# Optimization experiments

Hardware: AMD Instinct MI355X
Metric: run time of the kernel (lower is better)

Reference implementation:

```python
import jax, jax.numpy as jnp
import numpy as np

D_MODEL = 2048
N_HEADS = 16
HEAD_DIM = D_MODEL // N_HEADS
D_FF = 8192


def setup_inputs() -> dict:
    key = jax.random.key(0)
    ks = jax.random.split(key, 16)
    s = 0.02
    inp = {
        'x': jax.random.normal(ks[0], (2, 2048, D_MODEL), dtype=jnp.float32),
        'Wq': jax.random.normal(ks[1], (D_MODEL, D_MODEL), jnp.float32) * s,
        'bq': jnp.zeros((D_MODEL,), jnp.float32),
        'Wk': jax.random.normal(ks[2], (D_MODEL, D_MODEL), jnp.float32) * s,
        'bk': jnp.zeros((D_MODEL,), jnp.float32),
        'Wv': jax.random.normal(ks[3], (D_MODEL, D_MODEL), jnp.float32) * s,
        'bv': jnp.zeros((D_MODEL,), jnp.float32),
        'Wo': jax.random.normal(ks[4], (D_MODEL, D_MODEL), jnp.float32) * s,
        'bo': jnp.zeros((D_MODEL,), jnp.float32),
        'rotary': jax.random.normal(ks[5], (1, 1, HEAD_DIM), jnp.float32) * s,
        'norm1_w': jnp.ones((D_MODEL,), jnp.float32),
        'norm2_w': jnp.ones((D_MODEL,), jnp.float32),
        'W1': jax.random.normal(ks[6], (2 * D_FF, D_MODEL), jnp.float32) * s,
        'b1': jnp.zeros((2 * D_FF,), jnp.float32),
        'W2': jax.random.normal(ks[7], (D_MODEL, D_FF), jnp.float32) * s,
        'b2': jnp.zeros((D_MODEL,), jnp.float32),
    }
    return inp


def _rmsnorm(x, w, eps=1e-8):
    return w * (x * jax.lax.rsqrt(jnp.mean(x * x, axis=-1, keepdims=True) + eps))


def reference(x, Wq, bq, Wk, bk, Wv, bv, Wo, bo, rotary, norm1_w, norm2_w, W1, b1, W2, b2):
    B, S, _ = x.shape
    # --- attention block ---
    h = _rmsnorm(x, norm1_w)
    q = (h @ Wq.T + bq).reshape(B, S, N_HEADS, HEAD_DIM)
    k = (h @ Wk.T + bk).reshape(B, S, N_HEADS, HEAD_DIM)
    v = (h @ Wv.T + bv).reshape(B, S, N_HEADS, HEAD_DIM)
    q = q + rotary  # (1,1,head_dim) broadcast over batch, seq, heads
    scores = jnp.einsum('bqhd,bkhd->bhqk', q, k) / jnp.sqrt(jnp.float32(HEAD_DIM))
    attn = jax.nn.softmax(scores, axis=-1)
    o = jnp.einsum('bhqk,bkhd->bqhd', attn, v).reshape(B, S, D_MODEL)
    x = x + (o @ Wo.T + bo)
    # --- SwiGLU FFN block ---
    h2 = _rmsnorm(x, norm2_w)
    g = h2 @ W1.T + b1
    x1, x2 = g[..., :D_FF], g[..., D_FF:]
    ff = (x1 * jax.nn.silu(x2)) @ W2.T + b2
    return x + ff
```

## Files before the change

### kernel.cpp

```cpp
#include <hip/hip_runtime.h>
#include <hip/hip_bf16.h>

#define D_MODEL 2048
#define N_HEADS 16
#define HEAD_DIM 128
#define D_FF 8192
#define BATCH 2
#define SEQ 2048
#define M_TOK (BATCH * SEQ)
#define QKV_LD 6144
#define QSCALE 0.12751744f

typedef __attribute__((ext_vector_type(8))) short short8;
typedef __attribute__((ext_vector_type(4))) short short4v;
typedef __attribute__((ext_vector_type(4))) float f32x4;
typedef __attribute__((ext_vector_type(16))) float f32x16;
typedef __attribute__((ext_vector_type(2))) unsigned int uint2v;
typedef __attribute__((ext_vector_type(4))) unsigned int uint4v;

__device__ __forceinline__ unsigned short f2b(float f) {
  __hip_bfloat16 h = __float2bfloat16(f);
  return *reinterpret_cast<unsigned short*>(&h);
}
__device__ __forceinline__ float b2f(unsigned short u) {
  unsigned int x = ((unsigned int)u) << 16;
  return __uint_as_float(x);
}

__device__ __forceinline__ void gload_lds16(const void* gsrc, void* ldst) {
  __builtin_amdgcn_global_load_lds(
      (const __attribute__((address_space(1))) void*)gsrc,
      (__attribute__((address_space(3))) void*)ldst, 16, 0, 0);
}

__device__ __forceinline__ f32x16 mfma32(short8 a, short8 b, f32x16 c) {
  return __builtin_amdgcn_mfma_f32_32x32x16_bf16(a, b, c, 0, 0, 0);
}
__device__ __forceinline__ unsigned int cvtpk(float lo, float hi) {
  unsigned int r;
  asm("v_cvt_pk_bf16_f32 %0, %1, %2" : "=v"(r) : "v"(lo), "v"(hi));
  return r;
}
__device__ __forceinline__ uint2v plswap(unsigned int a, unsigned int b) {
  return __builtin_amdgcn_permlane32_swap(a, b, false, false);
}

__global__ __launch_bounds__(256)
void cvt_kernel(const float* __restrict__ src, unsigned short* __restrict__ dst,
                int nchunks, float scale) {
  int i = blockIdx.x * blockDim.x + threadIdx.x;
  int stride = gridDim.x * blockDim.x;
  for (int c = i; c < nchunks; c += stride) {
    const float4 a = *(const float4*)(src + (size_t)c * 8);
    const float4 b = *(const float4*)(src + (size_t)c * 8 + 4);
    short8 r;
    r[0] = f2b(a.x * scale); r[1] = f2b(a.y * scale);
    r[2] = f2b(a.z * scale); r[3] = f2b(a.w * scale);
    r[4] = f2b(b.x * scale); r[5] = f2b(b.y * scale);
    r[6] = f2b(b.z * scale); r[7] = f2b(b.w * scale);
    *(short8*)(dst + (size_t)c * 8) = r;
  }
}

__global__ __launch_bounds__(256)
void cvt_w1p_kernel(const float* __restrict__ src,
                    unsigned short* __restrict__ dst) {
  int i = blockIdx.x * blockDim.x + threadIdx.x;
  int stride = gridDim.x * blockDim.x;
  const int total = 2 * D_FF * (D_MODEL / 8);
  for (int c = i; c < total; c += stride) {
    int rp = c >> 8, col8 = c & 255;
    int b = rp >> 6, half = (rp >> 5) & 1;
    int rs = half * D_FF + b * 32 + (rp & 31);
    const float* s = src + (size_t)rs * D_MODEL + col8 * 8;
    const float4 a = *(const float4*)s;
    const float4 bb = *(const float4*)(s + 4);
    short8 r;
    r[0] = f2b(a.x); r[1] = f2b(a.y); r[2] = f2b(a.z); r[3] = f2b(a.w);
    r[4] = f2b(bb.x); r[5] = f2b(bb.y); r[6] = f2b(bb.z); r[7] = f2b(bb.w);
    *(short8*)(dst + (size_t)c * 8) = r;
  }
}

__global__ void permb1_kernel(const float* __restrict__ b1,
                              float* __restrict__ b1p) {
  int i = blockIdx.x * 256 + threadIdx.x;
  int b = i >> 6, half = (i >> 5) & 1;
  b1p[i] = b1[half * D_FF + b * 32 + (i & 31)];
}

__global__ void biasqkv_kernel(const float* __restrict__ bq,
                               const float* __restrict__ bk,
                               const float* __restrict__ bv,
                               const float* __restrict__ rot,
                               float* __restrict__ outp) {
  int i = blockIdx.x * 256 + threadIdx.x;
  float v;
  if (i < 2048) v = (bq[i] + rot[i & (HEAD_DIM - 1)]) * QSCALE;
  else if (i < 4096) v = bk[i - 2048];
  else v = bv[i - 4096];
  outp[i] = v;
}

__global__ __launch_bounds__(256)
void rmsnorm_kernel(const float* __restrict__ x, const float* __restrict__ wv,
                    unsigned short* __restrict__ outp) {
  const int row = blockIdx.x;
  const float* xr = x + (size_t)row * D_MODEL;
  const int base = threadIdx.x * 8;
  float4 a = *(const float4*)(xr + base);
  float4 c = *(const float4*)(xr + base + 4);
  float ss = a.x * a.x + a.y * a.y + a.z * a.z + a.w * a.w +
             c.x * c.x + c.y * c.y + c.z * c.z + c.w * c.w;
#pragma unroll
  for (int m = 1; m < 64; m <<= 1) ss += __shfl_xor(ss, m);
  __shared__ float red[4];
  if ((threadIdx.x & 63) == 0) red[threadIdx.x >> 6] = ss;
  __syncthreads();
  float tot = red[0] + red[1] + red[2] + red[3];
  float sc = rsqrtf(tot * (1.0f / D_MODEL) + 1e-8f);
  float4 w0 = *(const float4*)(wv + base);
  float4 w1 = *(const float4*)(wv + base + 4);
  short8 r;
  r[0] = f2b(a.x * sc * w0.x); r[1] = f2b(a.y * sc * w0.y);
  r[2] = f2b(a.z * sc * w0.z); r[3] = f2b(a.w * sc * w0.w);
  r[4] = f2b(c.x * sc * w1.x); r[5] = f2b(c.y * sc * w1.y);
  r[6] = f2b(c.z * sc * w1.z); r[7] = f2b(c.w * sc * w1.w);
  *(short8*)(outp + (size_t)row * D_MODEL + base) = r;
}

template <int MODE>
__global__ __launch_bounds__(512, 2)
void gemm_p8(const unsigned short* __restrict__ A, int lda,
             const unsigned short* __restrict__ W, int ldw,
             const float* __restrict__ bias, void* __restrict__ outp,
             int N, int K, size_t out_zstride) {
  __shared__ unsigned short AL[2][2][128 * 64];
  __shared__ unsigned short BL[2][2][128 * 64];
  const int t = threadIdx.x;
  const int l = t & 63, w = t >> 6;
  const int wm = w >> 2, wn = w & 3;
  const int ln = l & 31, hi = l >> 5;
  const int m0 = blockIdx.y << 8, n0 = blockIdx.x << 8;
  const int koff = blockIdx.z * K;

  const int r0 = t >> 3;
  const int cb16 = (t & 7) * 16;
  const int sel = ((cb16 ^ ((r0 & 7) << 4)) >> 1);
  const unsigned short* Abase = A + (size_t)m0 * lda + koff;
  const unsigned short* Wbase = W + (size_t)n0 * ldw + koff;
  const int d0e = t * 8, d1e = (t + 512) * 8;

#define STAGE(XL, Xb, ld, dd, h, ktd)                                        \
  do {                                                                       \
    const unsigned short* s_ =                                               \
        (Xb) + (size_t)((h) * 128 + r0) * (ld) + (ktd) * 64 + sel;           \
    gload_lds16(s_, &XL[dd][h][d0e]);                                        \
    gload_lds16(s_ + (size_t)64 * (ld), &XL[dd][h][d1e]);                    \
  } while (0)

  const int swz = (ln & 7) << 4;
  const int hb = wn >> 1;
  const int browb = ((wn & 1) * 64 + ln) * 128;

  f32x16 acc[4][2] = {};
  short8 bf[2][4];

#define READB(dd)                                                            \
  do {                                                                       \
    const char* Bb_ = (const char*)&BL[dd][hb][0];                           \
    _Pragma("unroll") for (int cb_ = 0; cb_ < 2; cb_++)                      \
      _Pragma("unroll") for (int ks_ = 0; ks_ < 4; ks_++)                    \
        bf[cb_][ks_] = *(const short8*)(Bb_ + browb + cb_ * 4096 +           \
                                        ((ks_ * 32 + hi * 16) ^ swz));       \
  } while (0)

#define PHASE2(dd, p, STAGE_STMT, VM_STMT)                                   \
  do {                                                                       \
    const char* Ab_ = (const char*)&AL[dd][p][0];                            \
    short8 af_[2][4];                                                        \
    if ((p) == 0) READB(dd);                                                 \
    _Pragma("unroll") for (int sb_ = 0; sb_ < 2; sb_++) {                    \
      _Pragma("unroll") for (int ks_ = 0; ks_ < 4; ks_++)                    \
        af_[sb_][ks_] = *(const short8*)(Ab_ +                               \
                                         (wm * 64 + sb_ * 32 + ln) * 128 +   \
                                         ((ks_ * 32 + hi * 16) ^ swz));      \
    }                                                                        \
    STAGE_STMT;                                                              \
    __builtin_amdgcn_sched_barrier(0);                                       \
    VM_STMT;                                                                 \
    __builtin_amdgcn_sched_barrier(0);                                       \
    __builtin_amdgcn_s_barrier();                                            \
    __builtin_amdgcn_sched_barrier(0);                                       \
    __builtin_amdgcn_s_setprio(1);                                           \
    _Pragma("unroll") for (int sb_ = 0; sb_ < 2; sb_++)                      \
      _Pragma("unroll") for (int cb_ = 0; cb_ < 2; cb_++)                    \
        _Pragma("unroll") for (int ks_ = 0; ks_ < 4; ks_++)                  \
          acc[2 * (p) + sb_][cb_] =                                          \
              mfma32(af_[sb_][ks_], bf[cb_][ks_], acc[2 * (p) + sb_][cb_]);  \
    __builtin_amdgcn_s_setprio(0);                                           \
    __builtin_amdgcn_sched_barrier(0);                                       \
    __builtin_amdgcn_s_barrier();                                            \
    __builtin_amdgcn_sched_barrier(0);                                       \
  } while (0)

  const int NT = K >> 6;

  STAGE(AL, Abase, lda, 0, 0, 0);
  STAGE(AL, Abase, lda, 0, 1, 0);
  STAGE(BL, Wbase, ldw, 0, 0, 0);
  STAGE(BL, Wbase, ldw, 0, 1, 0);
  STAGE(AL, Abase, lda, 1, 0, 1);
  STAGE(BL, Wbase, ldw, 1, 0, 1);
  asm volatile("s_waitcnt vmcnt(4)" ::: "memory");
  __builtin_amdgcn_sched_barrier(0);
  __builtin_amdgcn_s_barrier();
  __builtin_amdgcn_sched_barrier(0);

  for (int kt = 0; kt < NT; kt += 2) {
    PHASE2(0, 0,
           {
             if (kt + 1 < NT) {
               STAGE(BL, Wbase, ldw, 1, 1, kt + 1);
               STAGE(AL, Abase, lda, 1, 1, kt + 1);
             }
           },
           {});
    PHASE2(0, 1,
           {
             if (kt + 2 < NT) {
               STAGE(AL, Abase, lda, 0, 0, kt + 2);
               STAGE(BL, Wbase, ldw, 0, 0, kt + 2);
             }
           },
           {
             if (kt + 2 < NT)
               asm volatile("s_waitcnt vmcnt(4)" ::: "memory");
             else
               asm volatile("s_waitcnt vmcnt(0)" ::: "memory");
           });
    PHASE2(1, 0,
           {
             if (kt + 2 < NT) {
               STAGE(BL, Wbase, ldw, 0, 1, kt + 2);
               STAGE(AL, Abase, lda, 0, 1, kt + 2);
             }
           },
           {});
    PHASE2(1, 1,
           {
             if (kt + 3 < NT) {
               STAGE(AL, Abase, lda, 1, 0, kt + 3);
               STAGE(BL, Wbase, ldw, 1, 0, kt + 3);
             }
           },
           {
             if (kt + 3 < NT)
               asm volatile("s_waitcnt vmcnt(4)" ::: "memory");
             else
               asm volatile("s_waitcnt vmcnt(0)" ::: "memory");
           });
  }
#undef PHASE2
#undef READB
#undef STAGE

#pragma unroll
  for (int rb = 0; rb < 4; rb++) {
    const int rowb = m0 + (rb >> 1) * 128 + wm * 64 + (rb & 1) * 32 + 4 * hi;
    if (MODE == 3) {
      const int col0 = n0 + wn * 64 + ln;
      const float b1v = bias[col0];
      const float b2v = bias[col0 + 32];
      const int jout = (n0 >> 1) + wn * 32 + ln;
#pragma unroll
      for (int r = 0; r < 16; r++) {
        const int row = rowb + (r & 3) + 8 * (r >> 2);
        float x1 = acc[rb][0][r] + b1v;
        float x2 = acc[rb][1][r] + b2v;
        float sg = x2 * __builtin_amdgcn_rcpf(1.0f + __expf(-x2));
        ((unsigned short*)outp)[(size_t)row * (N >> 1) + jout] = f2b(x1 * sg);
      }
    } else {
#pragma unroll
      for (int cb = 0; cb < 2; cb++) {
        const int col = n0 + wn * 64 + cb * 32 + ln;
        const float bv = (MODE == 0) ? bias[col] : 0.0f;
#pragma unroll
        for (int r = 0; r < 16; r++) {
          const int row = rowb + (r & 3) + 8 * (r >> 2);
          const float vv = acc[rb][cb][r] + bv;
          if (MODE == 0)
            ((unsigned short*)outp)[(size_t)row * N + col] = f2b(vv);
          else
            ((float*)outp + blockIdx.z * out_zstride)[(size_t)row * N + col] = vv;
        }
      }
    }
  }
}

__global__ __launch_bounds__(256)
void vtrans_kernel(const unsigned short* __restrict__ qkv,
                   unsigned short* __restrict__ vt) {
  const int bh = blockIdx.y;
  const int b = bh >> 4, h = bh & 15;
  const int s0 = blockIdx.x * 32;
  __shared__ unsigned short tile[32][136];
  const int t = threadIdx.x;
  for (int i = 0; i < 2; i++) {
    int c = t + i * 256;
    int s = c >> 4, dc = c & 15;
    *(short8*)&tile[s][dc * 8] =
        *(const short8*)(qkv + (size_t)(b * SEQ + s0 + s) * QKV_LD + 4096 +
                         h * HEAD_DIM + dc * 8);
  }
  __syncthreads();
  const int d = t >> 1, sh = (t & 1) * 16;
  unsigned short* dst = vt + ((size_t)bh * HEAD_DIM + d) * SEQ + s0 + sh;
  short8 r0, r1;
#pragma unroll
  for (int j = 0; j < 8; j++) r0[j] = tile[sh + j][d];
#pragma unroll
  for (int j = 0; j < 8; j++) r1[j] = tile[sh + 8 + j][d];
  *(short8*)dst = r0;
  *(short8*)(dst + 8) = r1;
}

__global__ __launch_bounds__(512, 2)
void attn_kernel(const unsigned short* __restrict__ qkv,
                 const unsigned short* __restrict__ vt,
                 unsigned short* __restrict__ o) {
  const int bh = blockIdx.y;
  const int b = bh >> 4, h = bh & 15;
  const int q0 = blockIdx.x << 8;
  const int t = threadIdx.x, w = t >> 6, l = t & 63;
  const int ln = l & 31, hi = l >> 5;

  __shared__ unsigned short Ks[2][64 * 128];

  short8 qf[8];
  {
    const unsigned short* qb =
        qkv + (size_t)(b * SEQ + q0 + w * 32 + ln) * QKV_LD + h * HEAD_DIM +
        hi * 8;
#pragma unroll
    for (int sl = 0; sl < 8; sl++) qf[sl] = *(const short8*)(qb + sl * 16);
  }

  f32x16 oacc[4] = {};
  float mrow = -1e30f, lrow = 0.f;

  const unsigned short* kbase =
      qkv + (size_t)(b * SEQ) * QKV_LD + 2048 + h * HEAD_DIM;
  const unsigned short* vbase = vt + (size_t)bh * HEAD_DIM * SEQ;

#define STAGEK(buf, kv0_)                                                    \
  do {                                                                       \
    _Pragma("unroll") for (int i_ = 0; i_ < 2; i_++) {                       \
      int c_ = t + i_ * 512;                                                 \
      int row_ = c_ >> 4, dc_ = c_ & 15;                                     \
      int sel_ = ((dc_ * 16) ^ ((row_ & 7) << 4)) >> 1;                      \
      gload_lds16(kbase + (size_t)((kv0_) + row_) * QKV_LD + sel_,           \
                  &Ks[buf][c_ * 8]);                                         \
    }                                                                        \
  } while (0)

  STAGEK(0, 0);
  __syncthreads();

  for (int it = 0; it < SEQ / 64; ++it) {
    const int cur = it & 1;
    const int kv0 = it * 64;

    short8 vf[4][4];
#pragma unroll
    for (int db = 0; db < 4; db++)
#pragma unroll
      for (int ks = 0; ks < 4; ks++)
        vf[db][ks] = *(const short8*)(vbase + (size_t)(db * 32 + ln) * SEQ +
                                      kv0 + ks * 16 + hi * 8);

    if (it + 1 < SEQ / 64) STAGEK(cur ^ 1, kv0 + 64);

    const char* kb = (const char*)&Ks[cur][0];
    f32x16 s0 = {}, s1 = {};
    __builtin_amdgcn_s_setprio(1);
#pragma unroll
    for (int sl = 0; sl < 8; sl++) {
      const int cw = (sl * 32 + hi * 16) ^ ((ln & 7) << 4);
      short8 kf0 = *(const short8*)(kb + ln * 256 + cw);
      short8 kf1 = *(const short8*)(kb + (32 + ln) * 256 + cw);
      s0 = mfma32(kf0, qf[sl], s0);
      s1 = mfma32(kf1, qf[sl], s1);
    }
    __builtin_amdgcn_s_setprio(0);

    float mx = s0[0];
#pragma unroll
    for (int r = 1; r < 16; r++) mx = fmaxf(mx, s0[r]);
#pragma unroll
    for (int r = 0; r < 16; r++) mx = fmaxf(mx, s1[r]);
    {
      uint2v r2 = plswap(__float_as_uint(mx), __float_as_uint(mx));
      mx = fmaxf(__uint_as_float(r2[0]), __uint_as_float(r2[1]));
    }

    if (!__all(mx <= mrow + 8.f)) {
      float mnew = fmaxf(mrow, mx);
      float fs = exp2f(mrow - mnew);
      mrow = mnew;
      lrow *= fs;
#pragma unroll
      for (int db = 0; db < 4; db++)
#pragma unroll
        for (int r = 0; r < 16; r++) oacc[db][r] *= fs;
    }

    float p0[16], p1[16];
    float sum = 0.f;
#pragma unroll
    for (int r = 0; r < 16; r++) {
      p0[r] = exp2f(s0[r] - mrow);
      sum += p0[r];
    }
#pragma unroll
    for (int r = 0; r < 16; r++) {
      p1[r] = exp2f(s1[r] - mrow);
      sum += p1[r];
    }
    lrow += sum;

    uint4v pk[4];
#define PACKSUB(P, K0)                                                       \
  {                                                                          \
    unsigned int a_, b_;                                                     \
    uint2v r_;                                                               \
    a_ = cvtpk(P[0], P[1]); b_ = cvtpk(P[4], P[5]);                          \
    r_ = plswap(a_, b_); pk[K0][0] = r_[0]; pk[K0][2] = r_[1];               \
    a_ = cvtpk(P[2], P[3]); b_ = cvtpk(P[6], P[7]);                          \
    r_ = plswap(a_, b_); pk[K0][1] = r_[0]; pk[K0][3] = r_[1];               \
    a_ = cvtpk(P[8], P[9]); b_ = cvtpk(P[12], P[13]);                        \
    r_ = plswap(a_, b_); pk[K0 + 1][0] = r_[0]; pk[K0 + 1][2] = r_[1];       \
    a_ = cvtpk(P[10], P[11]); b_ = cvtpk(P[14], P[15]);                      \
    r_ = plswap(a_, b_); pk[K0 + 1][1] = r_[0]; pk[K0 + 1][3] = r_[1];       \
  }
    PACKSUB(p0, 0);
    PACKSUB(p1, 2);
#undef PACKSUB

    __builtin_amdgcn_s_setprio(1);
#pragma unroll
    for (int db = 0; db < 4; db++)
#pragma unroll
      for (int ks = 0; ks < 4; ks++)
        oacc[db] = mfma32(vf[db][ks], __builtin_bit_cast(short8, pk[ks]),
                          oacc[db]);
    __builtin_amdgcn_s_setprio(0);

    __syncthreads();
  }
#undef STAGEK

  {
    uint2v r2 = plswap(__float_as_uint(lrow), __float_as_uint(lrow));
    lrow = __uint_as_float(r2[0]) + __uint_as_float(r2[1]);
  }
  const float inv = 1.0f / lrow;
  unsigned short* ob = o + (size_t)(b * SEQ + q0 + w * 32 + ln) * D_MODEL +
                       h * HEAD_DIM + hi * 4;
#pragma unroll
  for (int db = 0; db < 4; db++)
#pragma unroll
    for (int r = 0; r < 4; r++) {
      short4v v4;
#pragma unroll
      for (int j = 0; j < 4; j++)
        v4[j] = (short)f2b(oacc[db][4 * r + j] * inv);
      *(short4v*)(ob + db * 32 + r * 8) = v4;
    }
}

__global__ __launch_bounds__(256)
void reduceo_kernel(const float* __restrict__ p0, const float* __restrict__ p1,
                    const float* __restrict__ bo, const float* __restrict__ x,
                    float* __restrict__ out) {
  size_t i = (size_t)blockIdx.x * 256 + threadIdx.x;
  float4 a = ((const float4*)p0)[i];
  float4 b = ((const float4*)p1)[i];
  float4 xx = ((const float4*)x)[i];
  float4 bb = ((const float4*)bo)[i & 511];
  float4 o;
  o.x = a.x + b.x + xx.x + bb.x;
  o.y = a.y + b.y + xx.y + bb.y;
  o.z = a.z + b.z + xx.z + bb.z;
  o.w = a.w + b.w + xx.w + bb.w;
  ((float4*)out)[i] = o;
}

__global__ __launch_bounds__(256)
void reduce2_kernel(const float* __restrict__ p0, const float* __restrict__ p1,
                    const float* __restrict__ b2, float* __restrict__ out) {
  size_t i = (size_t)blockIdx.x * 256 + threadIdx.x;
  float4 a = ((const float4*)p0)[i];
  float4 b = ((const float4*)p1)[i];
  float4 o = ((const float4*)out)[i];
  float4 bb = ((const float4*)b2)[i & 511];
  o.x += a.x + b.x + bb.x;
  o.y += a.y + b.y + bb.y;
  o.z += a.z + b.z + bb.z;
  o.w += a.w + b.w + bb.w;
  ((float4*)out)[i] = o;
}

extern "C" void kernel_launch(void* const* d_in, const int* in_sizes, int n_in,
                              void* d_out, int out_size, void* d_ws,
                              size_t ws_size, hipStream_t stream) {
  (void)in_sizes; (void)n_in; (void)out_size; (void)ws_size;
  const float* x   = (const float*)d_in[0];
  const float* Wq  = (const float*)d_in[1];
  const float* bq  = (const float*)d_in[2];
  const float* Wk  = (const float*)d_in[3];
  const float* bk  = (const float*)d_in[4];
  const float* Wv  = (const float*)d_in[5];
  const float* bv  = (const float*)d_in[6];
  const float* Wo  = (const float*)d_in[7];
  const float* bo  = (const float*)d_in[8];
  const float* rot = (const float*)d_in[9];
  const float* n1w = (const float*)d_in[10];
  const float* n2w = (const float*)d_in[11];
  const float* W1  = (const float*)d_in[12];
  const float* b1  = (const float*)d_in[13];
  const float* W2  = (const float*)d_in[14];
  const float* b2  = (const float*)d_in[15];
  float* out = (float*)d_out;
  char* ws = (char*)d_ws;

  const size_t SZ_D2  = (size_t)D_MODEL * D_MODEL * 2;
  const size_t SZ_ACT = (size_t)M_TOK * D_MODEL * 2;
  const size_t SZ_W1  = (size_t)2 * D_FF * D_MODEL * 2;
  const size_t SZ_W2  = (size_t)D_MODEL * D_FF * 2;
  const size_t SZ_G   = (size_t)M_TOK * 2 * D_FF * 2;

  size_t off = 0;
  auto alloc = [&](size_t sz) { size_t o = off; off += (sz + 255) & ~(size_t)255; return o; };
  unsigned short* wqkv_b = (unsigned short*)(ws + alloc(3 * SZ_D2));
  unsigned short* wo_b   = (unsigned short*)(ws + alloc(SZ_D2));
  unsigned short* w1_b   = (unsigned short*)(ws + alloc(SZ_W1));
  unsigned short* w2_b   = (unsigned short*)(ws + alloc(SZ_W2));
  float*          biasq  = (float*)(ws + alloc(QKV_LD * 4));
  float*          b1p    = (float*)(ws + alloc(2 * D_FF * 4));
  unsigned short* h2_b   = (unsigned short*)(ws + alloc(SZ_ACT));
  char* pool = ws + alloc(SZ_G);
  unsigned short* h_b   = (unsigned short*)(pool);
  unsigned short* qkv_b = (unsigned short*)(pool + SZ_ACT);
  unsigned short* vt_b  = (unsigned short*)(pool + 4 * SZ_ACT);
  unsigned short* o_b   = (unsigned short*)(pool + 5 * SZ_ACT);
  float* po0 = (float*)pool;
  float* po1 = po0 + (size_t)M_TOK * D_MODEL;
  unsigned short* ff_b  = (unsigned short*)(pool);
  float* p0 = (float*)ws;
  float* p1 = p0 + (size_t)M_TOK * D_MODEL;

  cvt_kernel<<<1024, 256, 0, stream>>>(Wq, wqkv_b, D_MODEL * D_MODEL / 8, QSCALE);
  cvt_kernel<<<1024, 256, 0, stream>>>(Wk, wqkv_b + (size_t)D_MODEL * D_MODEL, D_MODEL * D_MODEL / 8, 1.0f);
  cvt_kernel<<<1024, 256, 0, stream>>>(Wv, wqkv_b + (size_t)2 * D_MODEL * D_MODEL, D_MODEL * D_MODEL / 8, 1.0f);
  cvt_kernel<<<1024, 256, 0, stream>>>(Wo, wo_b, D_MODEL * D_MODEL / 8, 1.0f);
  cvt_w1p_kernel<<<2048, 256, 0, stream>>>(W1, w1_b);
  cvt_kernel<<<2048, 256, 0, stream>>>(W2, w2_b, D_MODEL * D_FF / 8, 1.0f);
  biasqkv_kernel<<<QKV_LD / 256, 256, 0, stream>>>(bq, bk, bv, rot, biasq);
  permb1_kernel<<<2 * D_FF / 256, 256, 0, stream>>>(b1, b1p);

  rmsnorm_kernel<<<M_TOK, 256, 0, stream>>>(x, n1w, h_b);

  gemm_p8<0><<<dim3(QKV_LD / 256, M_TOK / 256), 512, 0, stream>>>(
      h_b, D_MODEL, wqkv_b, D_MODEL, biasq, qkv_b, QKV_LD, D_MODEL, 0);

  vtrans_kernel<<<dim3(SEQ / 32, BATCH * N_HEADS), 256, 0, stream>>>(qkv_b, vt_b);
  attn_kernel<<<dim3(SEQ / 256, BATCH * N_HEADS), 512, 0, stream>>>(qkv_b, vt_b, o_b);

  gemm_p8<2><<<dim3(D_MODEL / 256, M_TOK / 256, 2), 512, 0, stream>>>(
      o_b, D_MODEL, wo_b, D_MODEL, nullptr, po0, D_MODEL, D_MODEL / 2,
      (size_t)M_TOK * D_MODEL);
  reduceo_kernel<<<(M_TOK * D_MODEL / 4) / 256, 256, 0, stream>>>(
      po0, po1, bo, x, out);

  rmsnorm_kernel<<<M_TOK, 256, 0, stream>>>(out, n2w, h2_b);

  gemm_p8<3><<<dim3(2 * D_FF / 256, M_TOK / 256), 512, 0, stream>>>(
      h2_b, D_MODEL, w1_b, D_MODEL, b1p, ff_b, 2 * D_FF, D_MODEL, 0);

  gemm_p8<2><<<dim3(D_MODEL / 256, M_TOK / 256, 2), 512, 0, stream>>>(
      ff_b, D_FF, w2_b, D_FF, nullptr, p0, D_MODEL, D_FF / 2,
      (size_t)M_TOK * D_MODEL);

  reduce2_kernel<<<(M_TOK * D_MODEL / 4) / 256, 256, 0, stream>>>(p0, p1, b2, out);
}
```

Measured before the change: 877.8 us.

## Store split-K partials in bf16, fuse residual-reduce with RMSNorm, merge weight casts

```diff
diff --git a/kernel.cpp b/kernel.cpp
--- a/kernel.cpp
+++ b/kernel.cpp
@@ -46,19 +46,33 @@
 }
 
 __global__ __launch_bounds__(256)
-void cvt_kernel(const float* __restrict__ src, unsigned short* __restrict__ dst,
-                int nchunks, float scale) {
-  int i = blockIdx.x * blockDim.x + threadIdx.x;
-  int stride = gridDim.x * blockDim.x;
-  for (int c = i; c < nchunks; c += stride) {
-    const float4 a = *(const float4*)(src + (size_t)c * 8);
-    const float4 b = *(const float4*)(src + (size_t)c * 8 + 4);
+void cvt_all_kernel(const float* __restrict__ Wq, const float* __restrict__ Wk,
+                    const float* __restrict__ Wv, const float* __restrict__ Wo,
+                    const float* __restrict__ W2w,
+                    unsigned short* __restrict__ wqkv,
+                    unsigned short* __restrict__ wo,
+                    unsigned short* __restrict__ w2) {
+  const int NC = (D_MODEL * D_MODEL) / 8;
+  const int TOT = 4 * NC + (D_MODEL * D_FF) / 8;
+  int i = blockIdx.x * 256 + threadIdx.x;
+  int stride = gridDim.x * 256;
+  for (int c = i; c < TOT; c += stride) {
+    const float* s;
+    unsigned short* d;
+    float sc = 1.0f;
+    if (c < NC) { s = Wq + (size_t)c * 8; d = wqkv + (size_t)c * 8; sc = QSCALE; }
+    else if (c < 2 * NC) { s = Wk + (size_t)(c - NC) * 8; d = wqkv + (size_t)c * 8; }
+    else if (c < 3 * NC) { s = Wv + (size_t)(c - 2 * NC) * 8; d = wqkv + (size_t)c * 8; }
+    else if (c < 4 * NC) { s = Wo + (size_t)(c - 3 * NC) * 8; d = wo + (size_t)(c - 3 * NC) * 8; }
+    else { s = W2w + (size_t)(c - 4 * NC) * 8; d = w2 + (size_t)(c - 4 * NC) * 8; }
+    const float4 a = *(const float4*)s;
+    const float4 b = *(const float4*)(s + 4);
     short8 r;
-    r[0] = f2b(a.x * scale); r[1] = f2b(a.y * scale);
-    r[2] = f2b(a.z * scale); r[3] = f2b(a.w * scale);
-    r[4] = f2b(b.x * scale); r[5] = f2b(b.y * scale);
-    r[6] = f2b(b.z * scale); r[7] = f2b(b.w * scale);
-    *(short8*)(dst + (size_t)c * 8) = r;
+    r[0] = f2b(a.x * sc); r[1] = f2b(a.y * sc);
+    r[2] = f2b(a.z * sc); r[3] = f2b(a.w * sc);
+    r[4] = f2b(b.x * sc); r[5] = f2b(b.y * sc);
+    r[6] = f2b(b.z * sc); r[7] = f2b(b.w * sc);
+    *(short8*)d = r;
   }
 }
 
@@ -293,7 +307,8 @@
           if (MODE == 0)
             ((unsigned short*)outp)[(size_t)row * N + col] = f2b(vv);
           else
-            ((float*)outp + blockIdx.z * out_zstride)[(size_t)row * N + col] = vv;
+            ((unsigned short*)outp + blockIdx.z * out_zstride)
+                [(size_t)row * N + col] = f2b(vv);
         }
       }
     }
@@ -482,35 +497,78 @@
 }
 
 __global__ __launch_bounds__(256)
-void reduceo_kernel(const float* __restrict__ p0, const float* __restrict__ p1,
-                    const float* __restrict__ bo, const float* __restrict__ x,
-                    float* __restrict__ out) {
-  size_t i = (size_t)blockIdx.x * 256 + threadIdx.x;
-  float4 a = ((const float4*)p0)[i];
-  float4 b = ((const float4*)p1)[i];
-  float4 xx = ((const float4*)x)[i];
-  float4 bb = ((const float4*)bo)[i & 511];
-  float4 o;
-  o.x = a.x + b.x + xx.x + bb.x;
-  o.y = a.y + b.y + xx.y + bb.y;
-  o.z = a.z + b.z + xx.z + bb.z;
-  o.w = a.w + b.w + xx.w + bb.w;
-  ((float4*)out)[i] = o;
+void reduceo_norm_kernel(const unsigned short* __restrict__ p0,
+                         const unsigned short* __restrict__ p1,
+                         const float* __restrict__ bo,
+                         const float* __restrict__ x,
+                         const float* __restrict__ n2w,
+                         float* __restrict__ out,
+                         unsigned short* __restrict__ h2) {
+  const int row = blockIdx.x;
+  const int base = threadIdx.x * 8;
+  const size_t off = (size_t)row * D_MODEL + base;
+  short8 a = *(const short8*)(p0 + off);
+  short8 b = *(const short8*)(p1 + off);
+  float4 x0 = *(const float4*)(x + off);
+  float4 x1 = *(const float4*)(x + off + 4);
+  float4 bo0 = *(const float4*)(bo + base);
+  float4 bo1 = *(const float4*)(bo + base + 4);
+  float o[8];
+  o[0] = b2f((unsigned short)a[0]) + b2f((unsigned short)b[0]) + x0.x + bo0.x;
+  o[1] = b2f((unsigned short)a[1]) + b2f((unsigned short)b[1]) + x0.y + bo0.y;
+  o[2] = b2f((unsigned short)a[2]) + b2f((unsigned short)b[2]) + x0.z + bo0.z;
+  o[3] = b2f((unsigned short)a[3]) + b2f((unsigned short)b[3]) + x0.w + bo0.w;
+  o[4] = b2f((unsigned short)a[4]) + b2f((unsigned short)b[4]) + x1.x + bo1.x;
+  o[5] = b2f((unsigned short)a[5]) + b2f((unsigned short)b[5]) + x1.y + bo1.y;
+  o[6] = b2f((unsigned short)a[6]) + b2f((unsigned short)b[6]) + x1.z + bo1.z;
+  o[7] = b2f((unsigned short)a[7]) + b2f((unsigned short)b[7]) + x1.w + bo1.w;
+  float4 w0, w1;
+  w0.x = o[0]; w0.y = o[1]; w0.z = o[2]; w0.w = o[3];
+  w1.x = o[4]; w1.y = o[5]; w1.z = o[6]; w1.w = o[7];
+  *(float4*)(out + off) = w0;
+  *(float4*)(out + off + 4) = w1;
+  float ss = 0.f;
+#pragma unroll
+  for (int j = 0; j < 8; j++) ss += o[j] * o[j];
+#pragma unroll
+  for (int m = 1; m < 64; m <<= 1) ss += __shfl_xor(ss, m);
+  __shared__ float red[4];
+  if ((threadIdx.x & 63) == 0) red[threadIdx.x >> 6] = ss;
+  __syncthreads();
+  float tot = red[0] + red[1] + red[2] + red[3];
+  float sc = rsqrtf(tot * (1.0f / D_MODEL) + 1e-8f);
+  float4 g0 = *(const float4*)(n2w + base);
+  float4 g1 = *(const float4*)(n2w + base + 4);
+  short8 r;
+  r[0] = f2b(o[0] * sc * g0.x); r[1] = f2b(o[1] * sc * g0.y);
+  r[2] = f2b(o[2] * sc * g0.z); r[3] = f2b(o[3] * sc * g0.w);
+  r[4] = f2b(o[4] * sc * g1.x); r[5] = f2b(o[5] * sc * g1.y);
+  r[6] = f2b(o[6] * sc * g1.z); r[7] = f2b(o[7] * sc * g1.w);
+  *(short8*)(h2 + off) = r;
 }
 
 __global__ __launch_bounds__(256)
-void reduce2_kernel(const float* __restrict__ p0, const float* __restrict__ p1,
+void reduce2_kernel(const unsigned short* __restrict__ p0,
+                    const unsigned short* __restrict__ p1,
                     const float* __restrict__ b2, float* __restrict__ out) {
   size_t i = (size_t)blockIdx.x * 256 + threadIdx.x;
-  float4 a = ((const float4*)p0)[i];
-  float4 b = ((const float4*)p1)[i];
-  float4 o = ((const float4*)out)[i];
-  float4 bb = ((const float4*)b2)[i & 511];
-  o.x += a.x + b.x + bb.x;
-  o.y += a.y + b.y + bb.y;
-  o.z += a.z + b.z + bb.z;
-  o.w += a.w + b.w + bb.w;
-  ((float4*)out)[i] = o;
+  const int col8 = (int)(i & 255) * 8;
+  short8 a = *(const short8*)(p0 + i * 8);
+  short8 b = *(const short8*)(p1 + i * 8);
+  float4 o0 = ((const float4*)out)[i * 2];
+  float4 o1 = ((const float4*)out)[i * 2 + 1];
+  float4 bb0 = *(const float4*)(b2 + col8);
+  float4 bb1 = *(const float4*)(b2 + col8 + 4);
+  o0.x += b2f((unsigned short)a[0]) + b2f((unsigned short)b[0]) + bb0.x;
+  o0.y += b2f((unsigned short)a[1]) + b2f((unsigned short)b[1]) + bb0.y;
+  o0.z += b2f((unsigned short)a[2]) + b2f((unsigned short)b[2]) + bb0.z;
+  o0.w += b2f((unsigned short)a[3]) + b2f((unsigned short)b[3]) + bb0.w;
+  o1.x += b2f((unsigned short)a[4]) + b2f((unsigned short)b[4]) + bb1.x;
+  o1.y += b2f((unsigned short)a[5]) + b2f((unsigned short)b[5]) + bb1.y;
+  o1.z += b2f((unsigned short)a[6]) + b2f((unsigned short)b[6]) + bb1.z;
+  o1.w += b2f((unsigned short)a[7]) + b2f((unsigned short)b[7]) + bb1.w;
+  ((float4*)out)[i * 2] = o0;
+  ((float4*)out)[i * 2 + 1] = o1;
 }
 
 extern "C" void kernel_launch(void* const* d_in, const int* in_sizes, int n_in,
@@ -556,18 +614,14 @@
   unsigned short* qkv_b = (unsigned short*)(pool + SZ_ACT);
   unsigned short* vt_b  = (unsigned short*)(pool + 4 * SZ_ACT);
   unsigned short* o_b   = (unsigned short*)(pool + 5 * SZ_ACT);
-  float* po0 = (float*)pool;
-  float* po1 = po0 + (size_t)M_TOK * D_MODEL;
+  unsigned short* po0 = (unsigned short*)pool;
+  unsigned short* po1 = po0 + (size_t)M_TOK * D_MODEL;
   unsigned short* ff_b  = (unsigned short*)(pool);
-  float* p0 = (float*)ws;
-  float* p1 = p0 + (size_t)M_TOK * D_MODEL;
-
-  cvt_kernel<<<1024, 256, 0, stream>>>(Wq, wqkv_b, D_MODEL * D_MODEL / 8, QSCALE);
-  cvt_kernel<<<1024, 256, 0, stream>>>(Wk, wqkv_b + (size_t)D_MODEL * D_MODEL, D_MODEL * D_MODEL / 8, 1.0f);
-  cvt_kernel<<<1024, 256, 0, stream>>>(Wv, wqkv_b + (size_t)2 * D_MODEL * D_MODEL, D_MODEL * D_MODEL / 8, 1.0f);
-  cvt_kernel<<<1024, 256, 0, stream>>>(Wo, wo_b, D_MODEL * D_MODEL / 8, 1.0f);
+  unsigned short* p0 = (unsigned short*)ws;
+  unsigned short* p1 = p0 + (size_t)M_TOK * D_MODEL;
+
+  cvt_all_kernel<<<2048, 256, 0, stream>>>(Wq, Wk, Wv, Wo, W2, wqkv_b, wo_b, w2_b);
   cvt_w1p_kernel<<<2048, 256, 0, stream>>>(W1, w1_b);
-  cvt_kernel<<<2048, 256, 0, stream>>>(W2, w2_b, D_MODEL * D_FF / 8, 1.0f);
   biasqkv_kernel<<<QKV_LD / 256, 256, 0, stream>>>(bq, bk, bv, rot, biasq);
   permb1_kernel<<<2 * D_FF / 256, 256, 0, stream>>>(b1, b1p);
 
@@ -582,10 +636,7 @@
   gemm_p8<2><<<dim3(D_MODEL / 256, M_TOK / 256, 2), 512, 0, stream>>>(
       o_b, D_MODEL, wo_b, D_MODEL, nullptr, po0, D_MODEL, D_MODEL / 2,
       (size_t)M_TOK * D_MODEL);
-  reduceo_kernel<<<(M_TOK * D_MODEL / 4) / 256, 256, 0, stream>>>(
-      po0, po1, bo, x, out);
-
-  rmsnorm_kernel<<<M_TOK, 256, 0, stream>>>(out, n2w, h2_b);
+  reduceo_norm_kernel<<<M_TOK, 256, 0, stream>>>(po0, po1, bo, x, n2w, out, h2_b);
 
   gemm_p8<3><<<dim3(2 * D_FF / 256, M_TOK / 256), 512, 0, stream>>>(
       h2_b, D_MODEL, w1_b, D_MODEL, b1p, ff_b, 2 * D_FF, D_MODEL, 0);
@@ -594,5 +645,5 @@
       ff_b, D_FF, w2_b, D_FF, nullptr, p0, D_MODEL, D_FF / 2,
       (size_t)M_TOK * D_MODEL);
 
-  reduce2_kernel<<<(M_TOK * D_MODEL / 4) / 256, 256, 0, stream>>>(p0, p1, b2, out);
-}
+  reduce2_kernel<<<(M_TOK * D_MODEL / 8) / 256, 256, 0, stream>>>(p0, p1, b2, out);
+}
```

After: 852.0 us. -2.9%, faster.
